# Kernel tuning notes

Measured on AMD Instinct MI355X. Metric: run time of the kernel, lower is better.

The kernel has to match this reference:

```python
import jax, jax.numpy as jnp
import numpy as np

D_MODEL, D_K, D_V, H, GRID = 512, 64, 64, 8, 196
B = 4


def setup_inputs() -> dict:
    key = jax.random.key(0)
    ks = jax.random.split(key, 12)
    s = 0.02
    return {
        "queries": jax.random.normal(ks[0], (B, GRID, D_MODEL), jnp.float32),
        "keys": jax.random.normal(ks[1], (B, GRID, D_MODEL), jnp.float32),
        "values": jax.random.normal(ks[2], (B, GRID, D_MODEL), jnp.float32),
        "Wq": jax.random.normal(ks[3], (H * D_K, D_MODEL), jnp.float32) * s,
        "bq": jnp.zeros((H * D_K,), jnp.float32),
        "Wk": jax.random.normal(ks[4], (H * D_K, D_MODEL), jnp.float32) * s,
        "bk": jnp.zeros((H * D_K,), jnp.float32),
        "Wv": jax.random.normal(ks[5], (H * D_V, D_MODEL), jnp.float32) * s,
        "bv": jnp.zeros((H * D_V,), jnp.float32),
        "Wo": jax.random.normal(ks[6], (D_MODEL, H * D_V), jnp.float32) * s,
        "bo": jnp.zeros((D_MODEL,), jnp.float32),
        "scale": jnp.ones((1, H, GRID, GRID), jnp.float32) / np.sqrt(D_K).astype(np.float32),
    }


def reference(queries, keys, values, Wq, bq, Wk, bk, Wv, bv, Wo, bo, scale):
    b, nq, _ = queries.shape
    nk = values.shape[1]
    # linear projections (torch nn.Linear: x @ W.T + b)
    q_sig = queries @ Wq.T + bq          # (b, nq, h*dk)
    k_p = keys @ Wk.T + bk               # (b, nk, h*dk)
    v_p = values @ Wv.T + bv             # (b, nk, h*dv)
    # elementwise q*k interaction (b, nq, nk, h*dk)
    att_e = q_sig[:, :, None, :] * k_p[:, None, :, :]
    # sigmoid-gated values
    v_g = jax.nn.sigmoid(att_e) * v_p[:, None, :, :]
    v = v_g.reshape(b, nq, nk, H, D_K).transpose(0, 3, 1, 2, 4)      # (b,h,nq,nk,dk)
    att = att_e.reshape(b, nq, nk, H, D_K).transpose(0, 3, 1, 2, 4)  # (b,h,nq,nk,dk)
    att = att.sum(-1) * scale            # (b,h,nq,nk)
    p = jax.nn.softmax(att, axis=-1)     # dropout is identity in eval mode
    # (att.unsqueeze(-2) @ v).squeeze(-2)
    image = jnp.einsum("bhqk,bhqkd->bhqd", p, v)
    image = image.transpose(0, 2, 1, 3).reshape(b, nq, H * D_V)
    out = image @ Wo.T + bo              # (b, nq, d_model)
    out = jax.nn.sigmoid(q_sig * out) * out
    return out
```

## Files before the change

### kernel.cpp

```cpp
#include <hip/hip_runtime.h>
#include <hip/hip_bf16.h>
#include <math.h>

#define NQ 196
#define BATCH 4
#define HD 512
#define NH 8
#define DK 64
#define MROWS 784
#define MPAD 832

typedef __attribute__((ext_vector_type(8))) short short8;
typedef __attribute__((ext_vector_type(4))) short short4v;
typedef __attribute__((ext_vector_type(4))) float float4v;

__device__ __forceinline__ float b2f(short s) {
  return __uint_as_float(((unsigned)(unsigned short)s) << 16);
}
__device__ __forceinline__ short f2b(float x) {
  return __builtin_bit_cast(short, __float2bfloat16(x));
}
__device__ __forceinline__ float fexp2(float x) {
  float r; asm("v_exp_f32 %0, %1" : "=v"(r) : "v"(x)); return r;
}
__device__ __forceinline__ float frcp(float x) {
  float r; asm("v_rcp_f32 %0, %1" : "=v"(r) : "v"(x)); return r;
}
__device__ __forceinline__ void cvt4(float4 v, short4v& hi, short4v& lo) {
  float x[4] = {v.x, v.y, v.z, v.w};
  #pragma unroll
  for (int i = 0; i < 4; ++i) {
    hi[i] = f2b(x[i]);
    lo[i] = f2b(x[i] - b2f(hi[i]));
  }
}
__device__ __forceinline__ void gload_lds16(const void* g, void* l) {
  __builtin_amdgcn_global_load_lds(
      (const __attribute__((address_space(1))) unsigned int*)g,
      (__attribute__((address_space(3))) unsigned int*)l, 16, 0, 0);
}

struct WSplitArgs { const float* src[4]; short* hi[4]; short* lo[4]; };

__global__ __launch_bounds__(256)
void wsplit_kernel(WSplitArgs a) {
  const int seg = blockIdx.x >> 7;
  const size_t off = (size_t)(blockIdx.x & 127) * 2048 + (size_t)threadIdx.x * 8;
  const float* src = a.src[seg] + off;
  float4 v0 = *(const float4*)(src);
  float4 v1 = *(const float4*)(src + 4);
  short4v h0, l0, h1, l1;
  cvt4(v0, h0, l0); cvt4(v1, h1, l1);
  short8 vh = {h0[0],h0[1],h0[2],h0[3],h1[0],h1[1],h1[2],h1[3]};
  short8 vl = {l0[0],l0[1],l0[2],l0[3],l1[0],l1[1],l1[2],l1[3]};
  *(short8*)(a.hi[seg] + off) = vh;
  *(short8*)(a.lo[seg] + off) = vl;
}

struct GemmArgs {
  const float* X[3]; const short* Wh[3]; const short* Wl[3]; const float* bias[3];
  float* Cf[3]; short* Ch[3]; short* Cl[3]; const float* gate[3];
};

__global__ __launch_bounds__(512)
void mgemm(GemmArgs p, int N, int K) {
  const int z = blockIdx.z;
  const float* __restrict__ X  = p.X[z];
  const short* __restrict__ Wh = p.Wh[z];
  const short* __restrict__ Wl = p.Wl[z];

  __shared__ short smem[20480];
  short* const A_ = smem;
  short* const B_ = smem + 4096;
  float* const redC = (float*)smem;

  const int t = threadIdx.x;
  const int g = t >> 8;
  const int tt = t & 255;
  const int ln = t & 63, lm = ln & 15, quad = ln >> 4;
  const int w = (t >> 6) & 3;
  const int m0 = blockIdx.x * 16, n0 = blockIdx.y * 64;
  const int kb = g << 8;

  const int aRow = (tt & 127) >> 3, aK = (tt & 7) << 2;
  const bool aload = tt < 128;
  const float* Ap = X + (size_t)(m0 + aRow) * K + kb + aK;
  const int aIdx = aRow * 32 + aK;
  const int bRow = tt >> 2, bK = (tt & 3) << 3;
  const short* Bph = Wh + (size_t)(n0 + bRow) * K + kb + bK;
  const short* Bpl = Wl + (size_t)(n0 + bRow) * K + kb + bK;

  const int wn = w << 4;
  float4v acc = {0.f, 0.f, 0.f, 0.f};

  const int T = 8;
  float4 ra = aload ? *(const float4*)Ap : make_float4(0.f,0.f,0.f,0.f);
  gload_lds16(Bph, &B_[(((g << 1) + 0) * 2 + 0) * 2048 + tt * 8]);
  gload_lds16(Bpl, &B_[(((g << 1) + 0) * 2 + 1) * 2048 + tt * 8]);
  if (aload) {
    short4v ahi, alo; cvt4(ra, ahi, alo);
    *(short4v*)&A_[(((g << 1) + 0) * 2 + 0) * 512 + aIdx] = ahi;
    *(short4v*)&A_[(((g << 1) + 0) * 2 + 1) * 512 + aIdx] = alo;
  }

  for (int kt = 0; kt < T; ++kt) {
    const int buf = kt & 1;
    __syncthreads();
    if (kt + 1 < T) {
      if (aload) ra = *(const float4*)(Ap + (size_t)(kt + 1) * 32);
      const int nb = buf ^ 1;
      gload_lds16(Bph + (size_t)(kt + 1) * 32, &B_[(((g << 1) + nb) * 2 + 0) * 2048 + tt * 8]);
      gload_lds16(Bpl + (size_t)(kt + 1) * 32, &B_[(((g << 1) + nb) * 2 + 1) * 2048 + tt * 8]);
    }
    const short* Ab = &A_[((g << 1) + buf) * 2 * 512];
    const short* Bb = &B_[((g << 1) + buf) * 2 * 2048];
    short8 fah = *(const short8*)&Ab[0 * 512 + lm * 32 + (quad << 3)];
    short8 fal = *(const short8*)&Ab[1 * 512 + lm * 32 + (quad << 3)];
    short8 fbh = *(const short8*)&Bb[0 * 2048 + (wn + lm) * 32 + (quad << 3)];
    short8 fbl = *(const short8*)&Bb[1 * 2048 + (wn + lm) * 32 + (quad << 3)];
    acc = __builtin_amdgcn_mfma_f32_16x16x32_bf16(fah, fbh, acc, 0,0,0);
    acc = __builtin_amdgcn_mfma_f32_16x16x32_bf16(fah, fbl, acc, 0,0,0);
    acc = __builtin_amdgcn_mfma_f32_16x16x32_bf16(fal, fbh, acc, 0,0,0);
    if (kt + 1 < T) {
      const int nb = buf ^ 1;
      if (aload) {
        short4v ahi, alo; cvt4(ra, ahi, alo);
        *(short4v*)&A_[(((g << 1) + nb) * 2 + 0) * 512 + aIdx] = ahi;
        *(short4v*)&A_[(((g << 1) + nb) * 2 + 1) * 512 + aIdx] = alo;
      }
    }
  }

  __syncthreads();
  if (g == 1) *(float4v*)&redC[tt * 4] = acc;
  __syncthreads();
  if (g == 0) {
    const float* bias = p.bias[z];
    const float* gate = p.gate[z];
    float* Cf = p.Cf[z]; short* Ch = p.Ch[z]; short* Cl = p.Cl[z];
    const int n = n0 + wn + lm;
    const float bv = bias[n];
    #pragma unroll
    for (int r = 0; r < 4; ++r) {
      const int m = m0 + (quad << 2) + r;
      float c = acc[r] + redC[tt * 4 + r] + bv;
      if (gate) {
        const float qg = gate[(size_t)m * N + n];
        c = __fdividef(c, 1.f + __expf(-qg * c));
      }
      if (Cf) Cf[(size_t)m * N + n] = c;
      if (Ch) {
        const short hi = f2b(c);
        Ch[(size_t)m * N + n] = hi;
        Cl[(size_t)m * N + n] = f2b(c - b2f(hi));
      }
    }
  }
}

__global__ __launch_bounds__(512)
void attn_fused(const short* __restrict__ qsh, const short* __restrict__ qsl,
                const short* __restrict__ ksh, const short* __restrict__ ksl,
                const float* __restrict__ qsg, const float* __restrict__ kpg,
                const float* __restrict__ vpg, const float* __restrict__ scg,
                float* __restrict__ img) {
  const int q0 = blockIdx.x * 16;
  const int h  = blockIdx.y;
  const int b  = blockIdx.z;
  const int t  = threadIdx.x;
  const int w = t >> 6, ln = t & 63;
  const int lm = ln & 15, quad = ln >> 4;
  const float L2E = 1.4426950408889634f;

  __shared__ float S[16][210];
  __shared__ float R[8][16][64];

  const size_t abase = ((size_t)(b * NQ) + q0 + lm) * HD + h * DK + (quad << 3);
  short8 ah0 = *(const short8*)(qsh + abase);
  short8 ah1 = *(const short8*)(qsh + abase + 32);
  short8 al0 = *(const short8*)(qsl + abase);
  short8 al1 = *(const short8*)(qsl + abase + 32);

  for (int nt = w; nt < 13; nt += 8) {
    const size_t bbase = ((size_t)(b * NQ) + nt * 16 + lm) * HD + h * DK + (quad << 3);
    short8 bh0 = *(const short8*)(ksh + bbase);
    short8 bh1 = *(const short8*)(ksh + bbase + 32);
    short8 bl0 = *(const short8*)(ksl + bbase);
    short8 bl1 = *(const short8*)(ksl + bbase + 32);
    float4v acc = {0.f, 0.f, 0.f, 0.f};
    acc = __builtin_amdgcn_mfma_f32_16x16x32_bf16(ah0, bh0, acc, 0,0,0);
    acc = __builtin_amdgcn_mfma_f32_16x16x32_bf16(ah1, bh1, acc, 0,0,0);
    acc = __builtin_amdgcn_mfma_f32_16x16x32_bf16(ah0, bl0, acc, 0,0,0);
    acc = __builtin_amdgcn_mfma_f32_16x16x32_bf16(ah1, bl1, acc, 0,0,0);
    acc = __builtin_amdgcn_mfma_f32_16x16x32_bf16(al0, bh0, acc, 0,0,0);
    acc = __builtin_amdgcn_mfma_f32_16x16x32_bf16(al1, bh1, acc, 0,0,0);
    #pragma unroll
    for (int r = 0; r < 4; ++r)
      S[(quad << 2) + r][nt * 16 + lm] = acc[r];
  }
  __syncthreads();

  for (int i = 0; i < 2; ++i) {
    const int rr = (w << 1) + i;
    const int q = q0 + rr;
    const bool qok = q < NQ;
    const float* srow = scg + ((size_t)h * NQ + (qok ? q : 0)) * NQ;
    float att[4];
    #pragma unroll
    for (int j = 0; j < 4; ++j) {
      const int c = ln + (j << 6);
      att[j] = -1e30f;
      if (c < NQ) att[j] = S[rr][c] * srow[c] * L2E;
    }
    float m = fmaxf(fmaxf(att[0], att[1]), fmaxf(att[2], att[3]));
    #pragma unroll
    for (int off = 32; off; off >>= 1) m = fmaxf(m, __shfl_xor(m, off, 64));
    float e[4], s = 0.f;
    #pragma unroll
    for (int j = 0; j < 4; ++j) { e[j] = fexp2(att[j] - m); s += e[j]; }
    #pragma unroll
    for (int off = 32; off; off >>= 1) s += __shfl_xor(s, off, 64);
    const float rinv = __fdividef(1.f, s);
    #pragma unroll
    for (int j = 0; j < 4; ++j) {
      const int c = ln + (j << 6);
      if (c < NQ) S[rr][c] = e[j] * rinv;
    }
  }
  __syncthreads();

  const int d = ln;
  const int kg = w;
  const int kbeg = (kg * 49) >> 1;
  const int kend = ((kg + 1) * 49) >> 1;
  const float LOG2E = 1.4426950408889634f;

  float nqs[16];
  #pragma unroll
  for (int qi = 0; qi < 16; ++qi) {
    const int row = min(b * NQ + q0 + qi, MROWS - 1);
    nqs[qi] = -qsg[(size_t)row * HD + h * DK + d] * LOG2E;
  }
  const float* kp = kpg + ((size_t)(b * NQ)) * HD + h * DK + d;
  const float* vp = vpg + ((size_t)(b * NQ)) * HD + h * DK + d;

  float acc[16];
  #pragma unroll
  for (int qi = 0; qi < 16; ++qi) acc[qi] = 0.f;

  for (int k = kbeg; k < kend; ++k) {
    const float kv = kp[(size_t)k * HD];
    const float vv = vp[(size_t)k * HD];
    #pragma unroll
    for (int qi = 0; qi < 16; ++qi) {
      const float e = fexp2(nqs[qi] * kv);
      const float g = vv * frcp(1.f + e);
      acc[qi] += S[qi][k] * g;
    }
  }
  #pragma unroll
  for (int qi = 0; qi < 16; ++qi) R[kg][qi][d] = acc[qi];
  __syncthreads();

  #pragma unroll
  for (int j = 0; j < 2; ++j) {
    const int idx = t + (j << 9);
    const int qi = idx >> 6, dd = idx & 63;
    const int q = q0 + qi;
    if (q < NQ) {
      float s = 0.f;
      #pragma unroll
      for (int kk = 0; kk < 8; ++kk) s += R[kk][qi][dd];
      img[((size_t)(b * NQ) + q) * HD + h * DK + dd] = s;
    }
  }
}

extern "C" void kernel_launch(void* const* d_in, const int* in_sizes, int n_in,
                              void* d_out, int out_size, void* d_ws, size_t ws_size,
                              hipStream_t stream) {
  const float* queries = (const float*)d_in[0];
  const float* keys    = (const float*)d_in[1];
  const float* values  = (const float*)d_in[2];
  const float* Wq = (const float*)d_in[3];
  const float* bq = (const float*)d_in[4];
  const float* Wk = (const float*)d_in[5];
  const float* bk = (const float*)d_in[6];
  const float* Wv = (const float*)d_in[7];
  const float* bv = (const float*)d_in[8];
  const float* Wo = (const float*)d_in[9];
  const float* bo = (const float*)d_in[10];
  const float* scale = (const float*)d_in[11];

  char* base = (char*)d_ws;
  const size_t FB = sizeof(float);
  const size_t NELF  = (size_t)MROWS * HD;
  const size_t NELPS = (size_t)MPAD * HD;
  const size_t WEL   = (size_t)HD * HD;

  size_t o = 0;
  float* q_sig = (float*)(base + o); o += NELF * FB;
  float* k_p   = (float*)(base + o); o += NELF * FB;
  float* v_p   = (float*)(base + o); o += NELF * FB;
  float* image = (float*)(base + o); o += NELF * FB;
  short* qsh = (short*)(base + o); o += NELPS * 2;
  short* qsl = (short*)(base + o); o += NELPS * 2;
  short* ksh = (short*)(base + o); o += NELPS * 2;
  short* ksl = (short*)(base + o); o += NELPS * 2;
  short* Wqh = (short*)(base + o); o += WEL * 2;
  short* Wql = (short*)(base + o); o += WEL * 2;
  short* Wkh = (short*)(base + o); o += WEL * 2;
  short* Wkl = (short*)(base + o); o += WEL * 2;
  short* Wvh = (short*)(base + o); o += WEL * 2;
  short* Wvl = (short*)(base + o); o += WEL * 2;
  short* Woh = (short*)(base + o); o += WEL * 2;
  short* Wol = (short*)(base + o); o += WEL * 2;

  WSplitArgs wa;
  wa.src[0] = Wq; wa.hi[0] = Wqh; wa.lo[0] = Wql;
  wa.src[1] = Wk; wa.hi[1] = Wkh; wa.lo[1] = Wkl;
  wa.src[2] = Wv; wa.hi[2] = Wvh; wa.lo[2] = Wvl;
  wa.src[3] = Wo; wa.hi[3] = Woh; wa.lo[3] = Wol;
  wsplit_kernel<<<512, 256, 0, stream>>>(wa);

  GemmArgs gp;
  gp.X[0] = queries; gp.Wh[0] = Wqh; gp.Wl[0] = Wql; gp.bias[0] = bq;
  gp.Cf[0] = q_sig;  gp.Ch[0] = qsh; gp.Cl[0] = qsl; gp.gate[0] = nullptr;
  gp.X[1] = keys;    gp.Wh[1] = Wkh; gp.Wl[1] = Wkl; gp.bias[1] = bk;
  gp.Cf[1] = k_p;    gp.Ch[1] = ksh; gp.Cl[1] = ksl; gp.gate[1] = nullptr;
  gp.X[2] = values;  gp.Wh[2] = Wvh; gp.Wl[2] = Wvl; gp.bias[2] = bv;
  gp.Cf[2] = v_p;    gp.Ch[2] = nullptr; gp.Cl[2] = nullptr; gp.gate[2] = nullptr;
  mgemm<<<dim3(MROWS/16, HD/64, 3), 512, 0, stream>>>(gp, HD, HD);

  attn_fused<<<dim3(13, NH, BATCH), 512, 0, stream>>>(
      qsh, qsl, ksh, ksl, q_sig, k_p, v_p, scale, image);

  GemmArgs go;
  go.X[0] = image; go.Wh[0] = Woh; go.Wl[0] = Wol; go.bias[0] = bo;
  go.Cf[0] = (float*)d_out; go.Ch[0] = nullptr; go.Cl[0] = nullptr; go.gate[0] = q_sig;
  for (int i = 1; i < 3; ++i) {
    go.X[i] = nullptr; go.Wh[i] = nullptr; go.Wl[i] = nullptr; go.bias[i] = nullptr;
    go.Cf[i] = nullptr; go.Ch[i] = nullptr; go.Cl[i] = nullptr; go.gate[i] = nullptr;
  }
  mgemm<<<dim3(MROWS/16, HD/64, 1), 512, 0, stream>>>(go, HD, HD);
}
```

Baseline: 138.5 us.

## Pre-split activations to bf16 hi/lo and retile GEMM to 64x64 swizzled tiles

Activations (queries/keys/values) are now split into bf16 hi/lo in the weight-split pass, and the attention kernel writes its output directly as hi/lo, so the GEMM loads both operands straight into LDS with swizzled 64x64 tiles and no in-kernel conversion or split-K reduction. The attention inner loop is unrolled by 4 with vectorized float4 reads of the score row and an even 24-key partition per warp. This trades extra global traffic for the pre-split buffers and an extra pass in the split kernel for higher per-block data reuse and fewer blocks. Reads into padded rows beyond 784 depend on the workspace padding.

```diff
diff --git a/kernel.cpp b/kernel.cpp
--- a/kernel.cpp
+++ b/kernel.cpp
@@ -40,12 +40,13 @@
       (__attribute__((address_space(3))) unsigned int*)l, 16, 0, 0);
 }
 
-struct WSplitArgs { const float* src[4]; short* hi[4]; short* lo[4]; };
+struct WSplitArgs { const float* src[7]; short* hi[7]; short* lo[7]; int nblk[7]; };
 
 __global__ __launch_bounds__(256)
 void wsplit_kernel(WSplitArgs a) {
-  const int seg = blockIdx.x >> 7;
-  const size_t off = (size_t)(blockIdx.x & 127) * 2048 + (size_t)threadIdx.x * 8;
+  int b = blockIdx.x, seg = 0;
+  while (seg < 6 && b >= a.nblk[seg]) { b -= a.nblk[seg]; ++seg; }
+  const size_t off = (size_t)b * 2048 + (size_t)threadIdx.x * 8;
   const float* src = a.src[seg] + off;
   float4 v0 = *(const float4*)(src);
   float4 v1 = *(const float4*)(src + 4);
@@ -58,101 +59,101 @@
 }
 
 struct GemmArgs {
-  const float* X[3]; const short* Wh[3]; const short* Wl[3]; const float* bias[3];
+  const short* Ah[3]; const short* Al[3];
+  const short* Bh[3]; const short* Bl[3];
+  const float* bias[3];
   float* Cf[3]; short* Ch[3]; short* Cl[3]; const float* gate[3];
 };
 
 __global__ __launch_bounds__(512)
-void mgemm(GemmArgs p, int N, int K) {
+void mgemm(GemmArgs p, int M, int N, int K) {
   const int z = blockIdx.z;
-  const float* __restrict__ X  = p.X[z];
-  const short* __restrict__ Wh = p.Wh[z];
-  const short* __restrict__ Wl = p.Wl[z];
-
-  __shared__ short smem[20480];
-  short* const A_ = smem;
-  short* const B_ = smem + 4096;
-  float* const redC = (float*)smem;
-
+  const short* __restrict__ Ah = p.Ah[z];
+  const short* __restrict__ Al = p.Al[z];
+  const short* __restrict__ Bh = p.Bh[z];
+  const short* __restrict__ Bl = p.Bl[z];
+
+  __shared__ short smem[32768];
   const int t = threadIdx.x;
-  const int g = t >> 8;
-  const int tt = t & 255;
   const int ln = t & 63, lm = ln & 15, quad = ln >> 4;
-  const int w = (t >> 6) & 3;
-  const int m0 = blockIdx.x * 16, n0 = blockIdx.y * 64;
-  const int kb = g << 8;
-
-  const int aRow = (tt & 127) >> 3, aK = (tt & 7) << 2;
-  const bool aload = tt < 128;
-  const float* Ap = X + (size_t)(m0 + aRow) * K + kb + aK;
-  const int aIdx = aRow * 32 + aK;
-  const int bRow = tt >> 2, bK = (tt & 3) << 3;
-  const short* Bph = Wh + (size_t)(n0 + bRow) * K + kb + bK;
-  const short* Bpl = Wl + (size_t)(n0 + bRow) * K + kb + bK;
-
-  const int wn = w << 4;
-  float4v acc = {0.f, 0.f, 0.f, 0.f};
-
-  const int T = 8;
-  float4 ra = aload ? *(const float4*)Ap : make_float4(0.f,0.f,0.f,0.f);
-  gload_lds16(Bph, &B_[(((g << 1) + 0) * 2 + 0) * 2048 + tt * 8]);
-  gload_lds16(Bpl, &B_[(((g << 1) + 0) * 2 + 1) * 2048 + tt * 8]);
-  if (aload) {
-    short4v ahi, alo; cvt4(ra, ahi, alo);
-    *(short4v*)&A_[(((g << 1) + 0) * 2 + 0) * 512 + aIdx] = ahi;
-    *(short4v*)&A_[(((g << 1) + 0) * 2 + 1) * 512 + aIdx] = alo;
-  }
-
-  for (int kt = 0; kt < T; ++kt) {
+  const int w = t >> 6;
+  const int wm = w >> 1, wn = w & 1;
+  const int m0 = blockIdx.x << 6, n0 = blockIdx.y << 6;
+
+  const int sr = t >> 3;
+  const int sc = ((t & 7) ^ (sr & 7)) << 3;
+  const short* gA_h = Ah + (size_t)(m0 + sr) * K + sc;
+  const short* gA_l = Al + (size_t)(m0 + sr) * K + sc;
+  const short* gB_h = Bh + (size_t)(n0 + sr) * K + sc;
+  const short* gB_l = Bl + (size_t)(n0 + sr) * K + sc;
+  const int ldst = t * 8;
+
+  float4v acc0 = {0.f,0.f,0.f,0.f}, acc1 = {0.f,0.f,0.f,0.f};
+
+  gload_lds16(gA_h, &smem[0     + ldst]);
+  gload_lds16(gA_l, &smem[4096  + ldst]);
+  gload_lds16(gB_h, &smem[8192  + ldst]);
+  gload_lds16(gB_l, &smem[12288 + ldst]);
+
+  const int NT = K >> 6;
+  const int ar = (wm << 4) + lm;
+  const int br0 = (wn << 5) + lm, br1 = br0 + 16;
+  const int swz = (lm & 7) << 3;
+
+  for (int kt = 0; kt < NT; ++kt) {
     const int buf = kt & 1;
     __syncthreads();
-    if (kt + 1 < T) {
-      if (aload) ra = *(const float4*)(Ap + (size_t)(kt + 1) * 32);
-      const int nb = buf ^ 1;
-      gload_lds16(Bph + (size_t)(kt + 1) * 32, &B_[(((g << 1) + nb) * 2 + 0) * 2048 + tt * 8]);
-      gload_lds16(Bpl + (size_t)(kt + 1) * 32, &B_[(((g << 1) + nb) * 2 + 1) * 2048 + tt * 8]);
-    }
-    const short* Ab = &A_[((g << 1) + buf) * 2 * 512];
-    const short* Bb = &B_[((g << 1) + buf) * 2 * 2048];
-    short8 fah = *(const short8*)&Ab[0 * 512 + lm * 32 + (quad << 3)];
-    short8 fal = *(const short8*)&Ab[1 * 512 + lm * 32 + (quad << 3)];
-    short8 fbh = *(const short8*)&Bb[0 * 2048 + (wn + lm) * 32 + (quad << 3)];
-    short8 fbl = *(const short8*)&Bb[1 * 2048 + (wn + lm) * 32 + (quad << 3)];
-    acc = __builtin_amdgcn_mfma_f32_16x16x32_bf16(fah, fbh, acc, 0,0,0);
-    acc = __builtin_amdgcn_mfma_f32_16x16x32_bf16(fah, fbl, acc, 0,0,0);
-    acc = __builtin_amdgcn_mfma_f32_16x16x32_bf16(fal, fbh, acc, 0,0,0);
-    if (kt + 1 < T) {
-      const int nb = buf ^ 1;
-      if (aload) {
-        short4v ahi, alo; cvt4(ra, ahi, alo);
-        *(short4v*)&A_[(((g << 1) + nb) * 2 + 0) * 512 + aIdx] = ahi;
-        *(short4v*)&A_[(((g << 1) + nb) * 2 + 1) * 512 + aIdx] = alo;
-      }
-    }
-  }
-
-  __syncthreads();
-  if (g == 1) *(float4v*)&redC[tt * 4] = acc;
-  __syncthreads();
-  if (g == 0) {
-    const float* bias = p.bias[z];
-    const float* gate = p.gate[z];
-    float* Cf = p.Cf[z]; short* Ch = p.Ch[z]; short* Cl = p.Cl[z];
-    const int n = n0 + wn + lm;
+    if (kt + 1 < NT) {
+      const int kb = (kt + 1) << 6;
+      short* nb = &smem[(buf ^ 1) << 14];
+      gload_lds16(gA_h + kb, nb + 0     + ldst);
+      gload_lds16(gA_l + kb, nb + 4096  + ldst);
+      gload_lds16(gB_h + kb, nb + 8192  + ldst);
+      gload_lds16(gB_l + kb, nb + 12288 + ldst);
+    }
+    const short* Sb = &smem[buf << 14];
+    #pragma unroll
+    for (int h = 0; h < 2; ++h) {
+      const int c = (h << 5) + (quad << 3);
+      const int cs = c ^ swz;
+      short8 a_h = *(const short8*)&Sb[         ar  * 64 + cs];
+      short8 a_l = *(const short8*)&Sb[4096  +  ar  * 64 + cs];
+      short8 b0h = *(const short8*)&Sb[8192  +  br0 * 64 + cs];
+      short8 b0l = *(const short8*)&Sb[12288 +  br0 * 64 + cs];
+      short8 b1h = *(const short8*)&Sb[8192  +  br1 * 64 + cs];
+      short8 b1l = *(const short8*)&Sb[12288 +  br1 * 64 + cs];
+      acc0 = __builtin_amdgcn_mfma_f32_16x16x32_bf16(a_h, b0h, acc0, 0,0,0);
+      acc0 = __builtin_amdgcn_mfma_f32_16x16x32_bf16(a_h, b0l, acc0, 0,0,0);
+      acc0 = __builtin_amdgcn_mfma_f32_16x16x32_bf16(a_l, b0h, acc0, 0,0,0);
+      acc1 = __builtin_amdgcn_mfma_f32_16x16x32_bf16(a_h, b1h, acc1, 0,0,0);
+      acc1 = __builtin_amdgcn_mfma_f32_16x16x32_bf16(a_h, b1l, acc1, 0,0,0);
+      acc1 = __builtin_amdgcn_mfma_f32_16x16x32_bf16(a_l, b1h, acc1, 0,0,0);
+    }
+  }
+
+  const float* bias = p.bias[z];
+  const float* gate = p.gate[z];
+  float* Cf = p.Cf[z]; short* Ch = p.Ch[z]; short* Cl = p.Cl[z];
+  #pragma unroll
+  for (int nf = 0; nf < 2; ++nf) {
+    const float4v a = nf ? acc1 : acc0;
+    const int n = n0 + (wn << 5) + (nf << 4) + lm;
     const float bv = bias[n];
     #pragma unroll
     for (int r = 0; r < 4; ++r) {
-      const int m = m0 + (quad << 2) + r;
-      float c = acc[r] + redC[tt * 4 + r] + bv;
-      if (gate) {
-        const float qg = gate[(size_t)m * N + n];
-        c = __fdividef(c, 1.f + __expf(-qg * c));
-      }
-      if (Cf) Cf[(size_t)m * N + n] = c;
-      if (Ch) {
-        const short hi = f2b(c);
-        Ch[(size_t)m * N + n] = hi;
-        Cl[(size_t)m * N + n] = f2b(c - b2f(hi));
+      const int m = m0 + (wm << 4) + (quad << 2) + r;
+      if (m < M) {
+        float c = a[r] + bv;
+        if (gate) {
+          const float qg = gate[(size_t)m * N + n];
+          c = __fdividef(c, 1.f + __expf(-qg * c));
+        }
+        if (Cf) Cf[(size_t)m * N + n] = c;
+        if (Ch) {
+          const short hi = f2b(c);
+          Ch[(size_t)m * N + n] = hi;
+          Cl[(size_t)m * N + n] = f2b(c - b2f(hi));
+        }
       }
     }
   }
@@ -163,7 +164,7 @@
                 const short* __restrict__ ksh, const short* __restrict__ ksl,
                 const float* __restrict__ qsg, const float* __restrict__ kpg,
                 const float* __restrict__ vpg, const float* __restrict__ scg,
-                float* __restrict__ img) {
+                short* __restrict__ imgh, short* __restrict__ imgl) {
   const int q0 = blockIdx.x * 16;
   const int h  = blockIdx.y;
   const int b  = blockIdx.z;
@@ -172,7 +173,7 @@
   const int lm = ln & 15, quad = ln >> 4;
   const float L2E = 1.4426950408889634f;
 
-  __shared__ float S[16][210];
+  __shared__ __align__(16) float S[16][212];
   __shared__ float R[8][16][64];
 
   const size_t abase = ((size_t)(b * NQ) + q0 + lm) * HD + h * DK + (quad << 3);
@@ -231,8 +232,8 @@
 
   const int d = ln;
   const int kg = w;
-  const int kbeg = (kg * 49) >> 1;
-  const int kend = ((kg + 1) * 49) >> 1;
+  const int kbeg = kg * 24;
+  const int kend = (kg == 7) ? 196 : kbeg + 24;
   const float LOG2E = 1.4426950408889634f;
 
   float nqs[16];
@@ -248,14 +249,22 @@
   #pragma unroll
   for (int qi = 0; qi < 16; ++qi) acc[qi] = 0.f;
 
-  for (int k = kbeg; k < kend; ++k) {
-    const float kv = kp[(size_t)k * HD];
-    const float vv = vp[(size_t)k * HD];
+  for (int k = kbeg; k < kend; k += 4) {
+    const float kv0 = kp[(size_t)(k + 0) * HD];
+    const float kv1 = kp[(size_t)(k + 1) * HD];
+    const float kv2 = kp[(size_t)(k + 2) * HD];
+    const float kv3 = kp[(size_t)(k + 3) * HD];
+    const float vv0 = vp[(size_t)(k + 0) * HD];
+    const float vv1 = vp[(size_t)(k + 1) * HD];
+    const float vv2 = vp[(size_t)(k + 2) * HD];
+    const float vv3 = vp[(size_t)(k + 3) * HD];
     #pragma unroll
     for (int qi = 0; qi < 16; ++qi) {
-      const float e = fexp2(nqs[qi] * kv);
-      const float g = vv * frcp(1.f + e);
-      acc[qi] += S[qi][k] * g;
+      const float4 s4 = *(const float4*)&S[qi][k];
+      acc[qi] += s4.x * (vv0 * frcp(1.f + fexp2(nqs[qi] * kv0)));
+      acc[qi] += s4.y * (vv1 * frcp(1.f + fexp2(nqs[qi] * kv1)));
+      acc[qi] += s4.z * (vv2 * frcp(1.f + fexp2(nqs[qi] * kv2)));
+      acc[qi] += s4.w * (vv3 * frcp(1.f + fexp2(nqs[qi] * kv3)));
     }
   }
   #pragma unroll
@@ -271,7 +280,10 @@
       float s = 0.f;
       #pragma unroll
       for (int kk = 0; kk < 8; ++kk) s += R[kk][qi][dd];
-      img[((size_t)(b * NQ) + q) * HD + h * DK + dd] = s;
+      const size_t o = ((size_t)(b * NQ) + q) * HD + h * DK + dd;
+      const short hi = f2b(s);
+      imgh[o] = hi;
+      imgl[o] = f2b(s - b2f(hi));
     }
   }
 }
@@ -302,11 +314,18 @@
   float* q_sig = (float*)(base + o); o += NELF * FB;
   float* k_p   = (float*)(base + o); o += NELF * FB;
   float* v_p   = (float*)(base + o); o += NELF * FB;
-  float* image = (float*)(base + o); o += NELF * FB;
   short* qsh = (short*)(base + o); o += NELPS * 2;
   short* qsl = (short*)(base + o); o += NELPS * 2;
   short* ksh = (short*)(base + o); o += NELPS * 2;
   short* ksl = (short*)(base + o); o += NELPS * 2;
+  short* imgh = (short*)(base + o); o += NELPS * 2;
+  short* imgl = (short*)(base + o); o += NELPS * 2;
+  short* xqh = (short*)(base + o); o += NELPS * 2;
+  short* xql = (short*)(base + o); o += NELPS * 2;
+  short* xkh = (short*)(base + o); o += NELPS * 2;
+  short* xkl = (short*)(base + o); o += NELPS * 2;
+  short* xvh = (short*)(base + o); o += NELPS * 2;
+  short* xvl = (short*)(base + o); o += NELPS * 2;
   short* Wqh = (short*)(base + o); o += WEL * 2;
   short* Wql = (short*)(base + o); o += WEL * 2;
   short* Wkh = (short*)(base + o); o += WEL * 2;
@@ -317,30 +336,34 @@
   short* Wol = (short*)(base + o); o += WEL * 2;
 
   WSplitArgs wa;
-  wa.src[0] = Wq; wa.hi[0] = Wqh; wa.lo[0] = Wql;
-  wa.src[1] = Wk; wa.hi[1] = Wkh; wa.lo[1] = Wkl;
-  wa.src[2] = Wv; wa.hi[2] = Wvh; wa.lo[2] = Wvl;
-  wa.src[3] = Wo; wa.hi[3] = Woh; wa.lo[3] = Wol;
-  wsplit_kernel<<<512, 256, 0, stream>>>(wa);
+  wa.src[0] = Wq;      wa.hi[0] = Wqh; wa.lo[0] = Wql; wa.nblk[0] = 128;
+  wa.src[1] = Wk;      wa.hi[1] = Wkh; wa.lo[1] = Wkl; wa.nblk[1] = 128;
+  wa.src[2] = Wv;      wa.hi[2] = Wvh; wa.lo[2] = Wvl; wa.nblk[2] = 128;
+  wa.src[3] = Wo;      wa.hi[3] = Woh; wa.lo[3] = Wol; wa.nblk[3] = 128;
+  wa.src[4] = queries; wa.hi[4] = xqh; wa.lo[4] = xql; wa.nblk[4] = 196;
+  wa.src[5] = keys;    wa.hi[5] = xkh; wa.lo[5] = xkl; wa.nblk[5] = 196;
+  wa.src[6] = values;  wa.hi[6] = xvh; wa.lo[6] = xvl; wa.nblk[6] = 196;
+  wsplit_kernel<<<1100, 256, 0, stream>>>(wa);
 
   GemmArgs gp;
-  gp.X[0] = queries; gp.Wh[0] = Wqh; gp.Wl[0] = Wql; gp.bias[0] = bq;
-  gp.Cf[0] = q_sig;  gp.Ch[0] = qsh; gp.Cl[0] = qsl; gp.gate[0] = nullptr;
-  gp.X[1] = keys;    gp.Wh[1] = Wkh; gp.Wl[1] = Wkl; gp.bias[1] = bk;
-  gp.Cf[1] = k_p;    gp.Ch[1] = ksh; gp.Cl[1] = ksl; gp.gate[1] = nullptr;
-  gp.X[2] = values;  gp.Wh[2] = Wvh; gp.Wl[2] = Wvl; gp.bias[2] = bv;
-  gp.Cf[2] = v_p;    gp.Ch[2] = nullptr; gp.Cl[2] = nullptr; gp.gate[2] = nullptr;
-  mgemm<<<dim3(MROWS/16, HD/64, 3), 512, 0, stream>>>(gp, HD, HD);
+  gp.Ah[0] = xqh; gp.Al[0] = xql; gp.Bh[0] = Wqh; gp.Bl[0] = Wql; gp.bias[0] = bq;
+  gp.Cf[0] = q_sig; gp.Ch[0] = qsh; gp.Cl[0] = qsl; gp.gate[0] = nullptr;
+  gp.Ah[1] = xkh; gp.Al[1] = xkl; gp.Bh[1] = Wkh; gp.Bl[1] = Wkl; gp.bias[1] = bk;
+  gp.Cf[1] = k_p; gp.Ch[1] = ksh; gp.Cl[1] = ksl; gp.gate[1] = nullptr;
+  gp.Ah[2] = xvh; gp.Al[2] = xvl; gp.Bh[2] = Wvh; gp.Bl[2] = Wvl; gp.bias[2] = bv;
+  gp.Cf[2] = v_p; gp.Ch[2] = nullptr; gp.Cl[2] = nullptr; gp.gate[2] = nullptr;
+  mgemm<<<dim3(MPAD/64, HD/64, 3), 512, 0, stream>>>(gp, MROWS, HD, HD);
 
   attn_fused<<<dim3(13, NH, BATCH), 512, 0, stream>>>(
-      qsh, qsl, ksh, ksl, q_sig, k_p, v_p, scale, image);
+      qsh, qsl, ksh, ksl, q_sig, k_p, v_p, scale, imgh, imgl);
 
   GemmArgs go;
-  go.X[0] = image; go.Wh[0] = Woh; go.Wl[0] = Wol; go.bias[0] = bo;
+  go.Ah[0] = imgh; go.Al[0] = imgl; go.Bh[0] = Woh; go.Bl[0] = Wol; go.bias[0] = bo;
   go.Cf[0] = (float*)d_out; go.Ch[0] = nullptr; go.Cl[0] = nullptr; go.gate[0] = q_sig;
   for (int i = 1; i < 3; ++i) {
-    go.X[i] = nullptr; go.Wh[i] = nullptr; go.Wl[i] = nullptr; go.bias[i] = nullptr;
-    go.Cf[i] = nullptr; go.Ch[i] = nullptr; go.Cl[i] = nullptr; go.gate[i] = nullptr;
-  }
-  mgemm<<<dim3(MROWS/16, HD/64, 1), 512, 0, stream>>>(go, HD, HD);
-}
+    go.Ah[i] = nullptr; go.Al[i] = nullptr; go.Bh[i] = nullptr; go.Bl[i] = nullptr;
+    go.bias[i] = nullptr; go.Cf[i] = nullptr; go.Ch[i] = nullptr; go.Cl[i] = nullptr;
+    go.gate[i] = nullptr;
+  }
+  mgemm<<<dim3(MPAD/64, HD/64, 1), 512, 0, stream>>>(go, MROWS, HD, HD);
+}
```

New measurement: 138.4 us. About the same (-0.1%).
